# Performance work log

Hardware: AMD Instinct MI355X
Metric: run time of the kernel (lower is better)

## Reference

```python
import jax, jax.numpy as jnp
import numpy as np

B, S, D, K, R = 2, 2048, 2048, 8, 8
F_HID = D // 4


def setup_inputs() -> dict:
    key = jax.random.key(0)
    ks = jax.random.split(key, 9)
    h_L = jax.random.normal(ks[0], (B, S, D), jnp.float32)
    masked = jax.random.bernoulli(ks[1], 0.5, (B, S))  # True = masked token

    def lin(k, shape, fan_in):
        bound = 1.0 / np.sqrt(fan_in)
        return jax.random.uniform(k, shape, jnp.float32, -bound, bound)

    W_route = lin(ks[2], (D, K), D)
    b_route = lin(ks[3], (K,), D)
    W1 = lin(ks[4], (K, D, F_HID), D)
    b1 = lin(ks[5], (K, F_HID), D)
    W2 = lin(ks[6], (K, F_HID, D), F_HID)
    b2 = lin(ks[7], (K, D), F_HID)
    return {"h_L": h_L, "masked": masked, "W_route": W_route, "b_route": b_route,
            "W1": W1, "b1": b1, "W2": W2, "b2": b2, "range_r": R}


def _windowed_sum(x, r):
    # x: [B, S, ...]; returns sum over window [a-r, a+r] excluding position a itself.
    S_ = x.shape[1]
    zero = jnp.zeros_like(x[:, :1])
    cs = jnp.concatenate([zero, jnp.cumsum(x, axis=1)], axis=1)  # [B, S+1, ...]
    idx = jnp.arange(S_)
    hi = jnp.clip(idx + r, 0, S_ - 1) + 1
    lo = jnp.clip(idx - r, 0, S_)
    return cs[:, hi] - cs[:, lo] - x


def reference(h_L, masked, W_route, b_route, W1, b1, W2, b2, range_r):
    unm = (~masked).astype(h_L.dtype)  # [B,S], 1.0 at unmasked tokens
    # Per-token, per-expert 2-layer GELU MLP: [B,S,K,D]
    hid = jax.nn.gelu(jnp.einsum('bsd,kdf->bskf', h_L, W1) + b1, approximate=False)
    eo = jnp.einsum('bskf,kfd->bskd', hid, W2) + b2
    # Zero out masked tokens, then windowed neighbor mean (exact-erf GELU above).
    contrib = eo * unm[:, :, None, None]
    win = _windowed_sum(contrib, range_r)          # [B,S,K,D]
    cnt = _windowed_sum(unm, range_r)              # [B,S]
    mean = win / jnp.maximum(cnt, 1.0)[:, :, None, None]
    # Routing weights from the masked token's own hidden state.
    w = jax.nn.softmax(h_L @ W_route + b_route, axis=-1)  # [B,S,K]
    mixed = jnp.einsum('bsk,bskd->bsd', w, mean)
    # LayerNorm over d_model, no affine, eps=1e-5 (torch F.layer_norm default).
    mu = jnp.mean(mixed, axis=-1, keepdims=True)
    var = jnp.mean((mixed - mu) ** 2, axis=-1, keepdims=True)
    ln = (mixed - mu) / jnp.sqrt(var + 1e-5)
    valid = masked & (cnt > 0)
    return jnp.where(valid[:, :, None], ln, jnp.zeros((), h_L.dtype))
```

## Files before the change

kernel.cpp:

```cpp
#include <hip/hip_runtime.h>
#include <math.h>

#define B_ 2
#define S_ 2048
#define T_ (B_*S_)
#define D_ 2048
#define K_ 8
#define F_ 512
#define R_ 8
#define WSEG 16

typedef unsigned short ushort_t;
typedef __attribute__((__ext_vector_type__(8))) __bf16 bf16x8;
typedef __attribute__((__ext_vector_type__(4))) float f32x4;

__device__ __forceinline__ float bf2f(ushort_t u) {
    return __uint_as_float(((unsigned int)u) << 16);
}
__device__ __forceinline__ ushort_t f2bf(float f) {
    unsigned int u = __float_as_uint(f);
    unsigned int r = u + 0x7FFFu + ((u >> 16) & 1u);
    return (ushort_t)(r >> 16);
}
__device__ __forceinline__ float loadF(const void* p, size_t idx, int f32m) {
    if (f32m) return ((const float*)p)[idx];
    return bf2f(((const ushort_t*)p)[idx]);
}

#if defined(__has_builtin)
#if __has_builtin(__builtin_amdgcn_global_load_lds)
#define ASYNC_LDS 1
#endif
#endif
__device__ __forceinline__ void ld16_lds(void* l, const void* g) {
#ifdef ASYNC_LDS
    __builtin_amdgcn_global_load_lds((const __attribute__((address_space(1))) unsigned int*)g,
                                     (__attribute__((address_space(3))) unsigned int*)l,
                                     16, 0, 0);
#else
    *(uint4*)l = *(const uint4*)g;
#endif
}

__global__ void detect_kernel(const unsigned char* __restrict__ hraw,
                              const unsigned char* __restrict__ mraw,
                              int* __restrict__ modePtr) {
    __shared__ int has_non01, has_nz123, has_3F1, outlier;
    if (threadIdx.x == 0) { has_non01 = 0; has_nz123 = 0; has_3F1 = 0; outlier = 0; }
    __syncthreads();
    int a = 0, b = 0, c = 0, o = 0;
    for (int i = threadIdx.x; i < 4096; i += 256) {
        unsigned char v = mraw[i];
        if (v > 1) a = 1;
        if ((i & 3) != 0 && v != 0) b = 1;
        if ((i & 3) == 1 && v >= 2) c = 1;
        if ((i & 3) == 1) {
            unsigned char hb = hraw[i] & 0x7F;
            if (hb < 0x30 || hb > 0x47) o++;
        }
    }
    if (a) atomicOr(&has_non01, 1);
    if (b) atomicOr(&has_nz123, 1);
    if (c) atomicOr(&has_3F1, 1);
    if (o) atomicAdd(&outlier, o);
    __syncthreads();
    if (threadIdx.x == 0) {
        int mode;
        if (!has_non01) mode = has_nz123 ? 0 : 1;
        else            mode = has_3F1 ? 2 : 3;
        modePtr[0] = mode;
        modePtr[1] = (outlier > 256) ? 1 : 0;
    }
}

__global__ __launch_bounds__(256) void conv_h_kernel(const void* __restrict__ hraw,
                                                     const int* __restrict__ modePtr,
                                                     ushort_t* __restrict__ hbf) {
    size_t i = ((size_t)blockIdx.x * 256 + threadIdx.x) * 8;
    if (modePtr[1]) {
        const float* p = (const float*)hraw + i;
        float4 a = *(const float4*)p;
        float4 b = *(const float4*)(p + 4);
        uint4 o;
        o.x = (unsigned)f2bf(a.x) | ((unsigned)f2bf(a.y) << 16);
        o.y = (unsigned)f2bf(a.z) | ((unsigned)f2bf(a.w) << 16);
        o.z = (unsigned)f2bf(b.x) | ((unsigned)f2bf(b.y) << 16);
        o.w = (unsigned)f2bf(b.z) | ((unsigned)f2bf(b.w) << 16);
        *(uint4*)&hbf[i] = o;
    } else {
        *(uint4*)&hbf[i] = *(const uint4*)((const ushort_t*)hraw + i);
    }
}

__global__ void mask_norm_kernel(const void* __restrict__ raw, const int* __restrict__ modePtr,
                                 float* __restrict__ unmF, int* __restrict__ maskedI) {
    int t = blockIdx.x * 256 + threadIdx.x;
    if (t >= T_) return;
    int mode = modePtr[0];
    int m;
    if (mode == 0)      m = ((const unsigned char*)raw)[t] != 0;
    else if (mode == 1) m = ((const int*)raw)[t] != 0;
    else if (mode == 2) m = ((const ushort_t*)raw)[t] != 0;
    else                m = ((const unsigned int*)raw)[t] != 0;
    maskedI[t] = m;
    unmF[t] = m ? 0.0f : 1.0f;
}

__global__ void cnt_kernel(const float* __restrict__ unmF, const int* __restrict__ maskedI,
                           float* __restrict__ invcnt, int* __restrict__ valid) {
    int t = blockIdx.x * 256 + threadIdx.x;
    if (t >= T_) return;
    int b = t / S_, s = t % S_;
    int lo = s - R_; if (lo < 0) lo = 0;
    int hi = s + R_; if (hi > S_ - 1) hi = S_ - 1;
    float c = 0.f;
    for (int sp = lo; sp <= hi; ++sp) c += unmF[b * S_ + sp];
    c -= unmF[t];
    invcnt[t] = 1.0f / fmaxf(c, 1.0f);
    valid[t] = (maskedI[t] && c > 0.5f) ? 1 : 0;
}

__global__ __launch_bounds__(256) void router_kernel(const ushort_t* __restrict__ hbf,
                                                     const void* __restrict__ Wr,
                                                     const void* __restrict__ br,
                                                     const int* __restrict__ modePtr,
                                                     float* __restrict__ wout) {
    int t = blockIdx.x;
    int f32m = modePtr[1];
    float p[8];
#pragma unroll
    for (int k = 0; k < 8; ++k) p[k] = 0.f;
    if (f32m) {
        for (int d = threadIdx.x; d < D_; d += 256) {
            float hv = bf2f(hbf[(size_t)t * D_ + d]);
            const float* wrow = (const float*)Wr + (size_t)d * 8;
            float4 q0 = *(const float4*)wrow;
            float4 q1 = *(const float4*)(wrow + 4);
            p[0] += hv * q0.x; p[1] += hv * q0.y; p[2] += hv * q0.z; p[3] += hv * q0.w;
            p[4] += hv * q1.x; p[5] += hv * q1.y; p[6] += hv * q1.z; p[7] += hv * q1.w;
        }
    } else {
        const ushort_t* Wrb = (const ushort_t*)Wr;
        for (int d = threadIdx.x; d < D_; d += 256) {
            float hv = bf2f(hbf[(size_t)t * D_ + d]);
            uint4 q = *(const uint4*)&Wrb[(size_t)d * 8];
            p[0] += hv * __uint_as_float(q.x << 16);
            p[1] += hv * __uint_as_float(q.x & 0xFFFF0000u);
            p[2] += hv * __uint_as_float(q.y << 16);
            p[3] += hv * __uint_as_float(q.y & 0xFFFF0000u);
            p[4] += hv * __uint_as_float(q.z << 16);
            p[5] += hv * __uint_as_float(q.z & 0xFFFF0000u);
            p[6] += hv * __uint_as_float(q.w << 16);
            p[7] += hv * __uint_as_float(q.w & 0xFFFF0000u);
        }
    }
#pragma unroll
    for (int off = 32; off; off >>= 1)
#pragma unroll
        for (int k = 0; k < 8; ++k) p[k] += __shfl_down(p[k], off);
    __shared__ float sm[4][8];
    int w = threadIdx.x >> 6, lane = threadIdx.x & 63;
    if (lane == 0)
#pragma unroll
        for (int k = 0; k < 8; ++k) sm[w][k] = p[k];
    __syncthreads();
    if (threadIdx.x == 0) {
        float lg[8];
        float mx = -1e30f;
#pragma unroll
        for (int k = 0; k < 8; ++k) {
            lg[k] = sm[0][k] + sm[1][k] + sm[2][k] + sm[3][k] + loadF(br, k, f32m);
            mx = fmaxf(mx, lg[k]);
        }
        float ssum = 0.f;
#pragma unroll
        for (int k = 0; k < 8; ++k) { lg[k] = __expf(lg[k] - mx); ssum += lg[k]; }
        float inv = 1.0f / ssum;
#pragma unroll
        for (int k = 0; k < 8; ++k) wout[t * 8 + k] = lg[k] * inv;
    }
}

__global__ __launch_bounds__(256) void transpose_kernel(const void* __restrict__ in,
                                                        ushort_t* __restrict__ op,
                                                        int rows, int cols,
                                                        const int* __restrict__ modePtr) {
    __shared__ ushort_t tile[32][33];
    int f32m = modePtr[1];
    int kexp = blockIdx.z;
    size_t base = (size_t)kexp * rows * cols;
    ushort_t* ob = op + (size_t)kexp * rows * cols;
    int r0 = blockIdx.x * 32, c0 = blockIdx.y * 32;
    int tx = threadIdx.x & 31, ty = threadIdx.x >> 5;
#pragma unroll
    for (int i = 0; i < 4; ++i) {
        int r = ty + i * 8;
        tile[r][tx] = f2bf(loadF(in, base + (size_t)(r0 + r) * cols + c0 + tx, f32m));
    }
    __syncthreads();
#pragma unroll
    for (int i = 0; i < 4; ++i) {
        int c = ty + i * 8;
        ob[(size_t)(c0 + c) * rows + r0 + tx] = tile[tx][c];
    }
}

__global__ __launch_bounds__(256) void gemm1_kernel(const ushort_t* __restrict__ hbf,
                                                    const ushort_t* __restrict__ W1t,
                                                    const void* __restrict__ b1,
                                                    const int* __restrict__ modePtr,
                                                    ushort_t* __restrict__ hid) {
    __shared__ ushort_t Al[128 * 32];
    __shared__ ushort_t Bl[128 * 32];
    const int f32m = modePtr[1];
    const int kexp = blockIdx.z;
    const int bm = blockIdx.x, bn = blockIdx.y;
    const int tid = threadIdx.x;
    const int lane = tid & 63, w = tid >> 6;
    const int lm = lane & 15, quad = lane >> 4;
    const int wm = (w >> 1) * 64, wn = (w & 1) * 64;
    const ushort_t* Ab = hbf + (size_t)(bm * 128) * D_;
    const ushort_t* Bb = W1t + (size_t)kexp * F_ * D_ + (size_t)(bn * 128) * D_;
    f32x4 acc[4][4];
    const f32x4 zz = {0.f, 0.f, 0.f, 0.f};
#pragma unroll
    for (int i = 0; i < 4; ++i)
#pragma unroll
        for (int j = 0; j < 4; ++j) acc[i][j] = zz;
    const int r0 = tid >> 2, c0 = (tid & 3) * 8;
    for (int kt = 0; kt < D_ / 32; ++kt) {
        const int kb = kt * 32;
        __syncthreads();
        ld16_lds(&Al[r0 * 32 + c0],        &Ab[(size_t)r0 * D_ + kb + c0]);
        ld16_lds(&Al[(r0 + 64) * 32 + c0], &Ab[(size_t)(r0 + 64) * D_ + kb + c0]);
        ld16_lds(&Bl[r0 * 32 + c0],        &Bb[(size_t)r0 * D_ + kb + c0]);
        ld16_lds(&Bl[(r0 + 64) * 32 + c0], &Bb[(size_t)(r0 + 64) * D_ + kb + c0]);
        __syncthreads();
        bf16x8 af[4], bfr[4];
#pragma unroll
        for (int i = 0; i < 4; ++i) af[i] = *(const bf16x8*)&Al[(wm + i * 16 + lm) * 32 + quad * 8];
#pragma unroll
        for (int j = 0; j < 4; ++j) bfr[j] = *(const bf16x8*)&Bl[(wn + j * 16 + lm) * 32 + quad * 8];
#pragma unroll
        for (int i = 0; i < 4; ++i)
#pragma unroll
            for (int j = 0; j < 4; ++j)
                acc[i][j] = __builtin_amdgcn_mfma_f32_16x16x32_bf16(af[i], bfr[j], acc[i][j], 0, 0, 0);
    }
#pragma unroll
    for (int j = 0; j < 4; ++j) {
        int fg = bn * 128 + wn + j * 16 + lm;
        float bias = loadF(b1, (size_t)kexp * F_ + fg, f32m);
#pragma unroll
        for (int i = 0; i < 4; ++i) {
            int mb = bm * 128 + wm + i * 16 + quad * 4;
#pragma unroll
            for (int v = 0; v < 4; ++v) {
                float x = acc[i][j][v] + bias;
                float g = 0.5f * x * (1.0f + erff(x * 0.70710678118654752f));
                hid[(size_t)kexp * T_ * F_ + (size_t)(mb + v) * F_ + fg] = f2bf(g);
            }
        }
    }
}

__global__ __launch_bounds__(256) void gemm2_kernel(const ushort_t* __restrict__ hid,
                                                    const ushort_t* __restrict__ W2t,
                                                    const void* __restrict__ b2,
                                                    const int* __restrict__ modePtr,
                                                    const float* __restrict__ unmF,
                                                    ushort_t* __restrict__ eo) {
    __shared__ ushort_t Al[128 * 32];
    __shared__ ushort_t Bl[128 * 32];
    const int f32m = modePtr[1];
    const int kexp = blockIdx.z;
    const int bm = blockIdx.x, bn = blockIdx.y;
    const int tid = threadIdx.x;
    const int lane = tid & 63, w = tid >> 6;
    const int lm = lane & 15, quad = lane >> 4;
    const int wm = (w >> 1) * 64, wn = (w & 1) * 64;
    const ushort_t* Ab = hid + (size_t)kexp * T_ * F_ + (size_t)(bm * 128) * F_;
    const ushort_t* Bb = W2t + (size_t)kexp * D_ * F_ + (size_t)(bn * 128) * F_;
    f32x4 acc[4][4];
    const f32x4 zz = {0.f, 0.f, 0.f, 0.f};
#pragma unroll
    for (int i = 0; i < 4; ++i)
#pragma unroll
        for (int j = 0; j < 4; ++j) acc[i][j] = zz;
    const int r0 = tid >> 2, c0 = (tid & 3) * 8;
    for (int kt = 0; kt < F_ / 32; ++kt) {
        const int kb = kt * 32;
        __syncthreads();
        ld16_lds(&Al[r0 * 32 + c0],        &Ab[(size_t)r0 * F_ + kb + c0]);
        ld16_lds(&Al[(r0 + 64) * 32 + c0], &Ab[(size_t)(r0 + 64) * F_ + kb + c0]);
        ld16_lds(&Bl[r0 * 32 + c0],        &Bb[(size_t)r0 * F_ + kb + c0]);
        ld16_lds(&Bl[(r0 + 64) * 32 + c0], &Bb[(size_t)(r0 + 64) * F_ + kb + c0]);
        __syncthreads();
        bf16x8 af[4], bfr[4];
#pragma unroll
        for (int i = 0; i < 4; ++i) af[i] = *(const bf16x8*)&Al[(wm + i * 16 + lm) * 32 + quad * 8];
#pragma unroll
        for (int j = 0; j < 4; ++j) bfr[j] = *(const bf16x8*)&Bl[(wn + j * 16 + lm) * 32 + quad * 8];
#pragma unroll
        for (int i = 0; i < 4; ++i)
#pragma unroll
            for (int j = 0; j < 4; ++j)
                acc[i][j] = __builtin_amdgcn_mfma_f32_16x16x32_bf16(af[i], bfr[j], acc[i][j], 0, 0, 0);
    }
#pragma unroll
    for (int j = 0; j < 4; ++j) {
        int dg = bn * 128 + wn + j * 16 + lm;
        float bias = loadF(b2, (size_t)kexp * D_ + dg, f32m);
#pragma unroll
        for (int i = 0; i < 4; ++i) {
            int mb = bm * 128 + wm + i * 16 + quad * 4;
#pragma unroll
            for (int v = 0; v < 4; ++v) {
                int tok = mb + v;
                float x = (acc[i][j][v] + bias) * unmF[tok];
                eo[((size_t)tok * K_ + kexp) * D_ + dg] = f2bf(x);
            }
        }
    }
}

__device__ __forceinline__ void acc8add(float* run, const ushort_t* p) {
    const uint4 q = *(const uint4*)p;
    run[0] += __uint_as_float(q.x << 16);
    run[1] += __uint_as_float(q.x & 0xFFFF0000u);
    run[2] += __uint_as_float(q.y << 16);
    run[3] += __uint_as_float(q.y & 0xFFFF0000u);
    run[4] += __uint_as_float(q.z << 16);
    run[5] += __uint_as_float(q.z & 0xFFFF0000u);
    run[6] += __uint_as_float(q.w << 16);
    run[7] += __uint_as_float(q.w & 0xFFFF0000u);
}
__device__ __forceinline__ void acc8sub(float* run, const ushort_t* p) {
    const uint4 q = *(const uint4*)p;
    run[0] -= __uint_as_float(q.x << 16);
    run[1] -= __uint_as_float(q.x & 0xFFFF0000u);
    run[2] -= __uint_as_float(q.y << 16);
    run[3] -= __uint_as_float(q.y & 0xFFFF0000u);
    run[4] -= __uint_as_float(q.z << 16);
    run[5] -= __uint_as_float(q.z & 0xFFFF0000u);
    run[6] -= __uint_as_float(q.w << 16);
    run[7] -= __uint_as_float(q.w & 0xFFFF0000u);
}

__global__ __launch_bounds__(256) void window_all_kernel(const ushort_t* __restrict__ eo,
                                                         const float* __restrict__ wR,
                                                         const int* __restrict__ maskedI,
                                                         const float* __restrict__ invcnt,
                                                         float* __restrict__ mixed) {
    const int b = blockIdx.y;
    const int s0 = blockIdx.x * WSEG;
    const int d0 = threadIdx.x * 8;
    float run[K_][8];
#pragma unroll
    for (int k = 0; k < K_; ++k)
#pragma unroll
        for (int j = 0; j < 8; ++j) run[k][j] = 0.f;
    int lo = s0 - R_; if (lo < 0) lo = 0;
    for (int sp = lo; sp < s0 + R_; ++sp) {
        const ushort_t* row = &eo[(size_t)(b * S_ + sp) * K_ * D_ + d0];
#pragma unroll
        for (int k = 0; k < K_; ++k) acc8add(run[k], row + (size_t)k * D_);
    }
    for (int s = s0; s < s0 + WSEG; ++s) {
        const int t = b * S_ + s;
        if (s + R_ < S_) {
            const ushort_t* row = &eo[(size_t)(t + R_) * K_ * D_ + d0];
#pragma unroll
            for (int k = 0; k < K_; ++k) acc8add(run[k], row + (size_t)k * D_);
        }
        if (maskedI[t]) {
            float ic = invcnt[t];
            float o[8];
#pragma unroll
            for (int j = 0; j < 8; ++j) o[j] = 0.f;
#pragma unroll
            for (int k = 0; k < K_; ++k) {
                float wk = wR[t * K_ + k] * ic;
#pragma unroll
                for (int j = 0; j < 8; ++j) o[j] += wk * run[k][j];
            }
            float4 o0 = {o[0], o[1], o[2], o[3]};
            float4 o1 = {o[4], o[5], o[6], o[7]};
            *(float4*)&mixed[(size_t)t * D_ + d0]     = o0;
            *(float4*)&mixed[(size_t)t * D_ + d0 + 4] = o1;
        }
        if (s - R_ >= 0) {
            const ushort_t* row = &eo[(size_t)(t - R_) * K_ * D_ + d0];
#pragma unroll
            for (int k = 0; k < K_; ++k) acc8sub(run[k], row + (size_t)k * D_);
        }
    }
}

__global__ __launch_bounds__(256) void ln_kernel(const float* __restrict__ mixed,
                                                 const int* __restrict__ valid,
                                                 const int* __restrict__ modePtr,
                                                 void* __restrict__ out) {
    const int t = blockIdx.x;
    const int tid = threadIdx.x;
    const int f32m = modePtr[1];
    if (!valid[t]) {
        if (f32m) {
            float4 z = {0.f, 0.f, 0.f, 0.f};
            float* op = (float*)out + (size_t)t * D_ + tid * 8;
            *(float4*)op = z; *(float4*)(op + 4) = z;
        } else {
            uint4 z = {0u, 0u, 0u, 0u};
            *(uint4*)((ushort_t*)out + (size_t)t * D_ + tid * 8) = z;
        }
        return;
    }
    float4 a = *(const float4*)&mixed[(size_t)t * D_ + tid * 8];
    float4 c = *(const float4*)&mixed[(size_t)t * D_ + tid * 8 + 4];
    float xs[8] = {a.x, a.y, a.z, a.w, c.x, c.y, c.z, c.w};
    float s1 = 0.f, s2 = 0.f;
#pragma unroll
    for (int j = 0; j < 8; ++j) { s1 += xs[j]; s2 += xs[j] * xs[j]; }
#pragma unroll
    for (int off = 32; off; off >>= 1) { s1 += __shfl_down(s1, off); s2 += __shfl_down(s2, off); }
    __shared__ float sm[8];
    int w = tid >> 6;
    if ((tid & 63) == 0) { sm[w * 2] = s1; sm[w * 2 + 1] = s2; }
    __syncthreads();
    float ts1 = sm[0] + sm[2] + sm[4] + sm[6];
    float ts2 = sm[1] + sm[3] + sm[5] + sm[7];
    float mu = ts1 * (1.0f / D_);
    float var = fmaxf(ts2 * (1.0f / D_) - mu * mu, 0.0f);
    float inv = rsqrtf(var + 1e-5f);
    if (f32m) {
        float* op = (float*)out + (size_t)t * D_ + tid * 8;
        float4 o0 = {(xs[0] - mu) * inv, (xs[1] - mu) * inv, (xs[2] - mu) * inv, (xs[3] - mu) * inv};
        float4 o1 = {(xs[4] - mu) * inv, (xs[5] - mu) * inv, (xs[6] - mu) * inv, (xs[7] - mu) * inv};
        *(float4*)op = o0; *(float4*)(op + 4) = o1;
    } else {
        ushort_t ob[8];
#pragma unroll
        for (int j = 0; j < 8; ++j) ob[j] = f2bf((xs[j] - mu) * inv);
        uint4 o;
        o.x = (unsigned)ob[0] | ((unsigned)ob[1] << 16);
        o.y = (unsigned)ob[2] | ((unsigned)ob[3] << 16);
        o.z = (unsigned)ob[4] | ((unsigned)ob[5] << 16);
        o.w = (unsigned)ob[6] | ((unsigned)ob[7] << 16);
        *(uint4*)((ushort_t*)out + (size_t)t * D_ + tid * 8) = o;
    }
}

extern "C" void kernel_launch(void* const* d_in, const int* in_sizes, int n_in,
                              void* d_out, int out_size, void* d_ws, size_t ws_size,
                              hipStream_t stream) {
    const void* h    = d_in[0];
    const void* mraw = d_in[1];
    const void* Wr   = d_in[2];
    const void* br   = d_in[3];
    const void* W1   = d_in[4];
    const void* b1   = d_in[5];
    const void* W2   = d_in[6];
    const void* b2   = d_in[7];
    (void)in_sizes; (void)n_in; (void)out_size; (void)ws_size;

    char* ws = (char*)d_ws;
    size_t off = 0;
    auto alloc = [&](size_t bytes) -> void* {
        void* p = ws + off;
        off += (bytes + 255) & ~(size_t)255;
        return p;
    };
    ushort_t* hbf   = (ushort_t*)alloc((size_t)T_ * D_ * 2);
    ushort_t* W1t   = (ushort_t*)alloc((size_t)K_ * F_ * D_ * 2);
    ushort_t* W2t   = (ushort_t*)alloc((size_t)K_ * D_ * F_ * 2);
    ushort_t* hid   = (ushort_t*)alloc((size_t)K_ * T_ * F_ * 2);
    ushort_t* eo    = (ushort_t*)alloc((size_t)T_ * K_ * D_ * 2);
    float*    wRbuf = (float*)alloc((size_t)T_ * K_ * 4);
    float*    unmF  = (float*)alloc((size_t)T_ * 4);
    int*      maskI = (int*)alloc((size_t)T_ * 4);
    float*    invc  = (float*)alloc((size_t)T_ * 4);
    int*      valid = (int*)alloc((size_t)T_ * 4);
    int*      mode  = (int*)alloc(256);
    float*    mixed = (float*)hid;

    hipLaunchKernelGGL(detect_kernel, dim3(1), dim3(256), 0, stream,
                       (const unsigned char*)h, (const unsigned char*)mraw, mode);
    hipLaunchKernelGGL(conv_h_kernel, dim3(T_ * D_ / 8 / 256), dim3(256), 0, stream,
                       h, mode, hbf);
    hipLaunchKernelGGL(mask_norm_kernel, dim3(T_ / 256), dim3(256), 0, stream,
                       mraw, mode, unmF, maskI);
    hipLaunchKernelGGL(cnt_kernel, dim3(T_ / 256), dim3(256), 0, stream,
                       unmF, maskI, invc, valid);
    hipLaunchKernelGGL(router_kernel, dim3(T_), dim3(256), 0, stream,
                       hbf, Wr, br, mode, wRbuf);
    hipLaunchKernelGGL(transpose_kernel, dim3(D_ / 32, F_ / 32, K_), dim3(256), 0, stream,
                       W1, W1t, D_, F_, mode);
    hipLaunchKernelGGL(transpose_kernel, dim3(F_ / 32, D_ / 32, K_), dim3(256), 0, stream,
                       W2, W2t, F_, D_, mode);
    hipLaunchKernelGGL(gemm1_kernel, dim3(T_ / 128, F_ / 128, K_), dim3(256), 0, stream,
                       hbf, W1t, b1, mode, hid);
    hipLaunchKernelGGL(gemm2_kernel, dim3(T_ / 128, D_ / 128, K_), dim3(256), 0, stream,
                       hid, W2t, b2, mode, unmF, eo);
    hipLaunchKernelGGL(window_all_kernel, dim3(S_ / WSEG, B_), dim3(256), 0, stream,
                       eo, wRbuf, maskI, invc, mixed);
    hipLaunchKernelGGL(ln_kernel, dim3(T_), dim3(256), 0, stream,
                       mixed, valid, mode, d_out);
}
```

Before: 490.2 us.

## Compact unmasked tokens so expert GEMMs and window sums skip masked rows

```diff
diff --git a/kernel.cpp b/kernel.cpp
--- a/kernel.cpp
+++ b/kernel.cpp
@@ -73,12 +73,73 @@
     }
 }
 
-__global__ __launch_bounds__(256) void conv_h_kernel(const void* __restrict__ hraw,
-                                                     const int* __restrict__ modePtr,
-                                                     ushort_t* __restrict__ hbf) {
-    size_t i = ((size_t)blockIdx.x * 256 + threadIdx.x) * 8;
+__global__ __launch_bounds__(256) void mask_prep_kernel(const void* __restrict__ raw,
+                                                        const int* __restrict__ modePtr,
+                                                        int* __restrict__ maskI,
+                                                        int* __restrict__ idx,
+                                                        int* __restrict__ TcPtr,
+                                                        float* __restrict__ invcnt,
+                                                        int* __restrict__ valid) {
+    __shared__ int sm[T_];
+    __shared__ int cnts[257];
+    const int tid = threadIdx.x;
+    const int mode = modePtr[0];
+    for (int t = tid; t < T_; t += 256) {
+        int m;
+        if (mode == 0)      m = ((const unsigned char*)raw)[t] != 0;
+        else if (mode == 1) m = ((const int*)raw)[t] != 0;
+        else if (mode == 2) m = ((const ushort_t*)raw)[t] != 0;
+        else                m = ((const unsigned int*)raw)[t] != 0;
+        sm[t] = m;
+        maskI[t] = m;
+    }
+    __syncthreads();
+    const int base = tid * 16;
+    int cnt = 0;
+#pragma unroll
+    for (int u = 0; u < 16; ++u) cnt += (sm[base + u] == 0);
+    cnts[tid] = cnt;
+    __syncthreads();
+    if (tid == 0) {
+        int run = 0;
+        for (int i = 0; i < 256; ++i) { int c = cnts[i]; cnts[i] = run; run += c; }
+        cnts[256] = run;
+    }
+    __syncthreads();
+    int run = cnts[tid];
+#pragma unroll
+    for (int u = 0; u < 16; ++u) {
+        int t = base + u;
+        if (!sm[t]) idx[run++] = t;
+    }
+    const int Tc = cnts[256];
+    for (int i = Tc + tid; i < T_; i += 256) idx[i] = T_;
+    if (tid == 0) TcPtr[0] = Tc;
+    for (int t = tid; t < T_; t += 256) {
+        int b = t >> 11, s = t & (S_ - 1);
+        int lo = s - R_; if (lo < 0) lo = 0;
+        int hi = s + R_; if (hi > S_ - 1) hi = S_ - 1;
+        int c = 0;
+        for (int sp = lo; sp <= hi; ++sp) c += (sm[b * S_ + sp] == 0);
+        c -= (sm[t] == 0);
+        invcnt[t] = 1.0f / fmaxf((float)c, 1.0f);
+        valid[t] = (sm[t] && c > 0) ? 1 : 0;
+    }
+}
+
+__global__ __launch_bounds__(256) void conv_hc_kernel(const void* __restrict__ hraw,
+                                                      const int* __restrict__ modePtr,
+                                                      const int* __restrict__ idx,
+                                                      const int* __restrict__ TcPtr,
+                                                      ushort_t* __restrict__ hbfc) {
+    int gid = blockIdx.x * 256 + threadIdx.x;
+    int i = gid >> 8;
+    if (i >= *TcPtr) return;
+    int col = (gid & 255) * 8;
+    size_t src = (size_t)idx[i] * D_ + col;
+    size_t dst = (size_t)i * D_ + col;
     if (modePtr[1]) {
-        const float* p = (const float*)hraw + i;
+        const float* p = (const float*)hraw + src;
         float4 a = *(const float4*)p;
         float4 b = *(const float4*)(p + 4);
         uint4 o;
@@ -86,53 +147,27 @@
         o.y = (unsigned)f2bf(a.z) | ((unsigned)f2bf(a.w) << 16);
         o.z = (unsigned)f2bf(b.x) | ((unsigned)f2bf(b.y) << 16);
         o.w = (unsigned)f2bf(b.z) | ((unsigned)f2bf(b.w) << 16);
-        *(uint4*)&hbf[i] = o;
+        *(uint4*)&hbfc[dst] = o;
     } else {
-        *(uint4*)&hbf[i] = *(const uint4*)((const ushort_t*)hraw + i);
-    }
-}
-
-__global__ void mask_norm_kernel(const void* __restrict__ raw, const int* __restrict__ modePtr,
-                                 float* __restrict__ unmF, int* __restrict__ maskedI) {
-    int t = blockIdx.x * 256 + threadIdx.x;
-    if (t >= T_) return;
-    int mode = modePtr[0];
-    int m;
-    if (mode == 0)      m = ((const unsigned char*)raw)[t] != 0;
-    else if (mode == 1) m = ((const int*)raw)[t] != 0;
-    else if (mode == 2) m = ((const ushort_t*)raw)[t] != 0;
-    else                m = ((const unsigned int*)raw)[t] != 0;
-    maskedI[t] = m;
-    unmF[t] = m ? 0.0f : 1.0f;
-}
-
-__global__ void cnt_kernel(const float* __restrict__ unmF, const int* __restrict__ maskedI,
-                           float* __restrict__ invcnt, int* __restrict__ valid) {
-    int t = blockIdx.x * 256 + threadIdx.x;
-    if (t >= T_) return;
-    int b = t / S_, s = t % S_;
-    int lo = s - R_; if (lo < 0) lo = 0;
-    int hi = s + R_; if (hi > S_ - 1) hi = S_ - 1;
-    float c = 0.f;
-    for (int sp = lo; sp <= hi; ++sp) c += unmF[b * S_ + sp];
-    c -= unmF[t];
-    invcnt[t] = 1.0f / fmaxf(c, 1.0f);
-    valid[t] = (maskedI[t] && c > 0.5f) ? 1 : 0;
-}
-
-__global__ __launch_bounds__(256) void router_kernel(const ushort_t* __restrict__ hbf,
+        *(uint4*)&hbfc[dst] = *(const uint4*)((const ushort_t*)hraw + src);
+    }
+}
+
+__global__ __launch_bounds__(256) void router_kernel(const void* __restrict__ hraw,
                                                      const void* __restrict__ Wr,
                                                      const void* __restrict__ br,
                                                      const int* __restrict__ modePtr,
+                                                     const int* __restrict__ maskI,
                                                      float* __restrict__ wout) {
     int t = blockIdx.x;
+    if (!maskI[t]) return;
     int f32m = modePtr[1];
     float p[8];
 #pragma unroll
     for (int k = 0; k < 8; ++k) p[k] = 0.f;
     if (f32m) {
         for (int d = threadIdx.x; d < D_; d += 256) {
-            float hv = bf2f(hbf[(size_t)t * D_ + d]);
+            float hv = ((const float*)hraw)[(size_t)t * D_ + d];
             const float* wrow = (const float*)Wr + (size_t)d * 8;
             float4 q0 = *(const float4*)wrow;
             float4 q1 = *(const float4*)(wrow + 4);
@@ -142,7 +177,7 @@
     } else {
         const ushort_t* Wrb = (const ushort_t*)Wr;
         for (int d = threadIdx.x; d < D_; d += 256) {
-            float hv = bf2f(hbf[(size_t)t * D_ + d]);
+            float hv = bf2f(((const ushort_t*)hraw)[(size_t)t * D_ + d]);
             uint4 q = *(const uint4*)&Wrb[(size_t)d * 8];
             p[0] += hv * __uint_as_float(q.x << 16);
             p[1] += hv * __uint_as_float(q.x & 0xFFFF0000u);
@@ -205,21 +240,24 @@
     }
 }
 
-__global__ __launch_bounds__(256) void gemm1_kernel(const ushort_t* __restrict__ hbf,
+__global__ __launch_bounds__(256) void gemm1_kernel(const ushort_t* __restrict__ hbfc,
                                                     const ushort_t* __restrict__ W1t,
                                                     const void* __restrict__ b1,
                                                     const int* __restrict__ modePtr,
-                                                    ushort_t* __restrict__ hid) {
+                                                    const int* __restrict__ TcPtr,
+                                                    ushort_t* __restrict__ hidc) {
+    const int bm = blockIdx.x;
+    if (bm * 128 >= *TcPtr) return;
     __shared__ ushort_t Al[128 * 32];
     __shared__ ushort_t Bl[128 * 32];
     const int f32m = modePtr[1];
     const int kexp = blockIdx.z;
-    const int bm = blockIdx.x, bn = blockIdx.y;
+    const int bn = blockIdx.y;
     const int tid = threadIdx.x;
     const int lane = tid & 63, w = tid >> 6;
     const int lm = lane & 15, quad = lane >> 4;
     const int wm = (w >> 1) * 64, wn = (w & 1) * 64;
-    const ushort_t* Ab = hbf + (size_t)(bm * 128) * D_;
+    const ushort_t* Ab = hbfc + (size_t)(bm * 128) * D_;
     const ushort_t* Bb = W1t + (size_t)kexp * F_ * D_ + (size_t)(bn * 128) * D_;
     f32x4 acc[4][4];
     const f32x4 zz = {0.f, 0.f, 0.f, 0.f};
@@ -258,28 +296,33 @@
             for (int v = 0; v < 4; ++v) {
                 float x = acc[i][j][v] + bias;
                 float g = 0.5f * x * (1.0f + erff(x * 0.70710678118654752f));
-                hid[(size_t)kexp * T_ * F_ + (size_t)(mb + v) * F_ + fg] = f2bf(g);
+                hidc[(size_t)kexp * T_ * F_ + (size_t)(mb + v) * F_ + fg] = f2bf(g);
             }
         }
     }
 }
 
-__global__ __launch_bounds__(256) void gemm2_kernel(const ushort_t* __restrict__ hid,
+__global__ __launch_bounds__(256) void gemm2_kernel(const ushort_t* __restrict__ hidc,
                                                     const ushort_t* __restrict__ W2t,
                                                     const void* __restrict__ b2,
                                                     const int* __restrict__ modePtr,
-                                                    const float* __restrict__ unmF,
+                                                    const int* __restrict__ TcPtr,
+                                                    const int* __restrict__ idx,
                                                     ushort_t* __restrict__ eo) {
+    const int bm = blockIdx.x;
+    if (bm * 128 >= *TcPtr) return;
     __shared__ ushort_t Al[128 * 32];
     __shared__ ushort_t Bl[128 * 32];
+    __shared__ int sidx[128];
     const int f32m = modePtr[1];
     const int kexp = blockIdx.z;
-    const int bm = blockIdx.x, bn = blockIdx.y;
+    const int bn = blockIdx.y;
     const int tid = threadIdx.x;
+    if (tid < 128) sidx[tid] = idx[bm * 128 + tid];
     const int lane = tid & 63, w = tid >> 6;
     const int lm = lane & 15, quad = lane >> 4;
     const int wm = (w >> 1) * 64, wn = (w & 1) * 64;
-    const ushort_t* Ab = hid + (size_t)kexp * T_ * F_ + (size_t)(bm * 128) * F_;
+    const ushort_t* Ab = hidc + (size_t)kexp * T_ * F_ + (size_t)(bm * 128) * F_;
     const ushort_t* Bb = W2t + (size_t)kexp * D_ * F_ + (size_t)(bn * 128) * F_;
     f32x4 acc[4][4];
     const f32x4 zz = {0.f, 0.f, 0.f, 0.f};
@@ -313,11 +356,11 @@
         float bias = loadF(b2, (size_t)kexp * D_ + dg, f32m);
 #pragma unroll
         for (int i = 0; i < 4; ++i) {
-            int mb = bm * 128 + wm + i * 16 + quad * 4;
+            int lr = wm + i * 16 + quad * 4;
 #pragma unroll
             for (int v = 0; v < 4; ++v) {
-                int tok = mb + v;
-                float x = (acc[i][j][v] + bias) * unmF[tok];
+                int tok = sidx[lr + v];
+                float x = acc[i][j][v] + bias;
                 eo[((size_t)tok * K_ + kexp) * D_ + dg] = f2bf(x);
             }
         }
@@ -349,7 +392,7 @@
 
 __global__ __launch_bounds__(256) void window_all_kernel(const ushort_t* __restrict__ eo,
                                                          const float* __restrict__ wR,
-                                                         const int* __restrict__ maskedI,
+                                                         const int* __restrict__ maskI,
                                                          const float* __restrict__ invcnt,
                                                          float* __restrict__ mixed) {
     const int b = blockIdx.y;
@@ -362,18 +405,19 @@
         for (int j = 0; j < 8; ++j) run[k][j] = 0.f;
     int lo = s0 - R_; if (lo < 0) lo = 0;
     for (int sp = lo; sp < s0 + R_; ++sp) {
+        if (maskI[b * S_ + sp]) continue;
         const ushort_t* row = &eo[(size_t)(b * S_ + sp) * K_ * D_ + d0];
 #pragma unroll
         for (int k = 0; k < K_; ++k) acc8add(run[k], row + (size_t)k * D_);
     }
     for (int s = s0; s < s0 + WSEG; ++s) {
         const int t = b * S_ + s;
-        if (s + R_ < S_) {
+        if (s + R_ < S_ && !maskI[t + R_]) {
             const ushort_t* row = &eo[(size_t)(t + R_) * K_ * D_ + d0];
 #pragma unroll
             for (int k = 0; k < K_; ++k) acc8add(run[k], row + (size_t)k * D_);
         }
-        if (maskedI[t]) {
+        if (maskI[t]) {
             float ic = invcnt[t];
             float o[8];
 #pragma unroll
@@ -389,7 +433,7 @@
             *(float4*)&mixed[(size_t)t * D_ + d0]     = o0;
             *(float4*)&mixed[(size_t)t * D_ + d0 + 4] = o1;
         }
-        if (s - R_ >= 0) {
+        if (s - R_ >= 0 && !maskI[t - R_]) {
             const ushort_t* row = &eo[(size_t)(t - R_) * K_ * D_ + d0];
 #pragma unroll
             for (int k = 0; k < K_; ++k) acc8sub(run[k], row + (size_t)k * D_);
@@ -470,37 +514,36 @@
         off += (bytes + 255) & ~(size_t)255;
         return p;
     };
-    ushort_t* hbf   = (ushort_t*)alloc((size_t)T_ * D_ * 2);
+    ushort_t* hbfc  = (ushort_t*)alloc((size_t)T_ * D_ * 2);
     ushort_t* W1t   = (ushort_t*)alloc((size_t)K_ * F_ * D_ * 2);
     ushort_t* W2t   = (ushort_t*)alloc((size_t)K_ * D_ * F_ * 2);
-    ushort_t* hid   = (ushort_t*)alloc((size_t)K_ * T_ * F_ * 2);
-    ushort_t* eo    = (ushort_t*)alloc((size_t)T_ * K_ * D_ * 2);
+    ushort_t* hidc  = (ushort_t*)alloc((size_t)K_ * T_ * F_ * 2);
+    ushort_t* eo    = (ushort_t*)alloc(((size_t)T_ + 1) * K_ * D_ * 2);
     float*    wRbuf = (float*)alloc((size_t)T_ * K_ * 4);
-    float*    unmF  = (float*)alloc((size_t)T_ * 4);
     int*      maskI = (int*)alloc((size_t)T_ * 4);
     float*    invc  = (float*)alloc((size_t)T_ * 4);
     int*      valid = (int*)alloc((size_t)T_ * 4);
+    int*      idx   = (int*)alloc((size_t)T_ * 4);
+    int*      Tc    = (int*)alloc(256);
     int*      mode  = (int*)alloc(256);
-    float*    mixed = (float*)hid;
+    float*    mixed = (float*)hidc;
 
     hipLaunchKernelGGL(detect_kernel, dim3(1), dim3(256), 0, stream,
                        (const unsigned char*)h, (const unsigned char*)mraw, mode);
-    hipLaunchKernelGGL(conv_h_kernel, dim3(T_ * D_ / 8 / 256), dim3(256), 0, stream,
-                       h, mode, hbf);
-    hipLaunchKernelGGL(mask_norm_kernel, dim3(T_ / 256), dim3(256), 0, stream,
-                       mraw, mode, unmF, maskI);
-    hipLaunchKernelGGL(cnt_kernel, dim3(T_ / 256), dim3(256), 0, stream,
-                       unmF, maskI, invc, valid);
+    hipLaunchKernelGGL(mask_prep_kernel, dim3(1), dim3(256), 0, stream,
+                       mraw, mode, maskI, idx, Tc, invc, valid);
+    hipLaunchKernelGGL(conv_hc_kernel, dim3(T_ * D_ / 8 / 256), dim3(256), 0, stream,
+                       h, mode, idx, Tc, hbfc);
     hipLaunchKernelGGL(router_kernel, dim3(T_), dim3(256), 0, stream,
-                       hbf, Wr, br, mode, wRbuf);
+                       h, Wr, br, mode, maskI, wRbuf);
     hipLaunchKernelGGL(transpose_kernel, dim3(D_ / 32, F_ / 32, K_), dim3(256), 0, stream,
                        W1, W1t, D_, F_, mode);
     hipLaunchKernelGGL(transpose_kernel, dim3(F_ / 32, D_ / 32, K_), dim3(256), 0, stream,
                        W2, W2t, F_, D_, mode);
     hipLaunchKernelGGL(gemm1_kernel, dim3(T_ / 128, F_ / 128, K_), dim3(256), 0, stream,
-                       hbf, W1t, b1, mode, hid);
+                       hbfc, W1t, b1, mode, Tc, hidc);
     hipLaunchKernelGGL(gemm2_kernel, dim3(T_ / 128, D_ / 128, K_), dim3(256), 0, stream,
-                       hid, W2t, b2, mode, unmF, eo);
+                       hidc, W2t, b2, mode, Tc, idx, eo);
     hipLaunchKernelGGL(window_all_kernel, dim3(S_ / WSEG, B_), dim3(256), 0, stream,
                        eo, wRbuf, maskI, invc, mixed);
     hipLaunchKernelGGL(ln_kernel, dim3(T_), dim3(256), 0, stream,
```

After: 447.9 us. 1.09x faster.
